# Performance work log

Hardware: AMD Instinct MI355X
Metric: run time of the kernel (lower is better)

Reference implementation:

```python
import jax, jax.numpy as jnp
import numpy as np

INT4_QMAX = 7.0  # symmetric int4: representable range clipped to [-8, 7]


def simulate_quantize_int4(w):
    # axis_to_reduce=None -> single global scale over the whole kernel
    scale = jnp.max(jnp.abs(w)) / INT4_QMAX
    q = jnp.clip(jnp.round(w / scale), -8.0, 7.0)
    return q * scale


def setup_inputs() -> dict:
    key = jax.random.key(0)
    k_x, k_w, k_bias, k_a, k_b = jax.random.split(key, 5)
    d_in, features, rank = 1024, 1024, 16
    x = jax.random.normal(k_x, (4, 8192, d_in), dtype=jnp.float32)
    kernel = jax.random.normal(k_w, (d_in, features), dtype=jnp.float32)
    bias = jax.random.normal(k_bias, (features,), dtype=jnp.float32)
    a = jax.random.normal(k_a, (d_in, rank), dtype=jnp.float32) * (1.0 / np.sqrt(d_in))
    b = jax.random.normal(k_b, (rank, features), dtype=jnp.float32) * 0.01
    return {"x": x, "kernel": kernel, "bias": bias, "a": a, "b": b}


def reference(x, kernel, bias, a, b):
    # fake-quantized main matmul: y = x @ dequant(quant(W)) + bias
    w = simulate_quantize_int4(kernel)
    y = jnp.einsum('bsd,df->bsf', x, w) + bias
    # LoRA adapter: x @ a @ b (contract small rank dim first)
    lora = jnp.einsum('bsr,rf->bsf', jnp.einsum('bsd,dr->bsr', x, a), b)
    return y + lora
```

## Files before the change

kernel.cpp:

```cpp
#include <hip/hip_runtime.h>
#include <hip/hip_bf16.h>

typedef __bf16 bf16x8 __attribute__((ext_vector_type(8)));
typedef __bf16 bf16x4 __attribute__((ext_vector_type(4)));
typedef float  f32x4  __attribute__((ext_vector_type(4)));

#define K_DIM 1024
#define N_DIM 1024
#define BM 128
#define BN 128
#define BK 64
#define BM2 256
#define BN2 256
#define BK2 32
#define NT2 (K_DIM / BK2)
#define AS_T (BM2 * BK2)
#define BS_T (BN2 * BK2)

typedef unsigned int u32;
typedef u32 __attribute__((address_space(1))) u32_g;
typedef u32 __attribute__((address_space(3))) u32_s;

__device__ __forceinline__ void load16_lds(const void* g, void* s) {
    __builtin_amdgcn_global_load_lds((u32_g*)g, (u32_s*)s, 16, 0, 0);
}

__global__ void maxabs_kernel(const float* __restrict__ w, float* __restrict__ blockmax, int n4) {
    __shared__ float sm[4];
    int i = blockIdx.x * blockDim.x + threadIdx.x;
    int stride = gridDim.x * blockDim.x;
    float m = 0.f;
    for (; i < n4; i += stride) {
        float4 v = ((const float4*)w)[i];
        m = fmaxf(m, fmaxf(fmaxf(fabsf(v.x), fabsf(v.y)), fmaxf(fabsf(v.z), fabsf(v.w))));
    }
#pragma unroll
    for (int off = 32; off > 0; off >>= 1)
        m = fmaxf(m, __shfl_down(m, off, 64));
    int lane = threadIdx.x & 63, wave = threadIdx.x >> 6;
    if (lane == 0) sm[wave] = m;
    __syncthreads();
    if (threadIdx.x == 0)
        blockmax[blockIdx.x] = fmaxf(fmaxf(sm[0], sm[1]), fmaxf(sm[2], sm[3]));
}

__global__ void build_w_kernel(const float* __restrict__ kern, const float* __restrict__ amat,
                               const float* __restrict__ bmat, const float* __restrict__ blockmax,
                               __bf16* __restrict__ wt) {
    __shared__ float smax;
    if (threadIdx.x < 64) {
        float m = 0.f;
#pragma unroll
        for (int j = 0; j < 4; ++j) m = fmaxf(m, blockmax[threadIdx.x + j * 64]);
#pragma unroll
        for (int off = 32; off > 0; off >>= 1)
            m = fmaxf(m, __shfl_down(m, off, 64));
        if (threadIdx.x == 0) smax = m;
    }
    __syncthreads();
    float scale = smax * (1.0f / 7.0f);

    int t = blockIdx.x * blockDim.x + threadIdx.x;
    int k = t & (K_DIM - 1);
    int n = t >> 10;
    float w = kern[k * N_DIM + n];
    float q = rintf(w / scale);
    q = fminf(fmaxf(q, -8.f), 7.f);
    float acc = q * scale;
#pragma unroll
    for (int r = 0; r < 16; ++r)
        acc += amat[k * 16 + r] * bmat[r * N_DIM + n];
    wt[(size_t)n * K_DIM + k] = (__bf16)acc;
}

__global__ __launch_bounds__(512, 2)
void gemm256_kernel(const float* __restrict__ x, const __bf16* __restrict__ wt,
                    const float* __restrict__ bias, float* __restrict__ out) {
    __shared__ __attribute__((aligned(16))) __bf16 As[2][AS_T];
    __shared__ __attribute__((aligned(16))) __bf16 Bs[4][BS_T];

    const int tid  = threadIdx.x;
    const int lane = tid & 63;
    const int wave = tid >> 6;
    const int wr   = wave >> 2;
    const int wc   = wave & 3;
    const int l15  = lane & 15;
    const int l4   = lane >> 4;

    const int lb  = blockIdx.x;
    const int ib  = lb >> 3;
    const int bn0 = (ib & 3) * BN2;
    const int bm0 = (((ib >> 2) << 3) | (lb & 7)) * BM2;

    const int srow = lane >> 2;
    const int lc   = (lane & 3) ^ ((srow >> 1) & 3);
    const __bf16* wg = wt + (size_t)(bn0 + wave * 32 + srow) * K_DIM + lc * 8;
    __bf16* sb = &Bs[0][wave * 32 * BK2];

    const int r0  = tid >> 3;
    const int c4  = tid & 7;
    const int apc = (c4 >> 1) ^ ((r0 >> 1) & 3);
    const int awr = r0 * BK2 + apc * 8 + (c4 & 1) * 4;
    const float* ag = x + (size_t)(bm0 + r0) * K_DIM + c4 * 4;

    const int ro = l15 * BK2 + ((l4 ^ ((l15 >> 1) & 3)) << 3);

    f32x4 acc[8][4] = {};
    float4 av0, av1, av2, av3;

#define STAGE_B(T) do { int b_ = (T) & 3; int k_ = ((T) & 31) * BK2;        \
        load16_lds(wg + k_,              sb + b_ * BS_T);                   \
        load16_lds(wg + 16 * K_DIM + k_, sb + b_ * BS_T + 16 * BK2); } while (0)

#define LOADA(T) do { const float* p_ = ag + ((T) & 31) * BK2;              \
        av0 = *(const float4*)(p_);                                         \
        av1 = *(const float4*)(p_ +  64 * K_DIM);                           \
        av2 = *(const float4*)(p_ + 128 * K_DIM);                           \
        av3 = *(const float4*)(p_ + 192 * K_DIM); } while (0)

#define WRITEA(T) do { __bf16* d_ = &As[(T) & 1][awr];                      \
        bf16x4 o0, o1, o2, o3;                                              \
        o0.x=(__bf16)av0.x; o0.y=(__bf16)av0.y; o0.z=(__bf16)av0.z; o0.w=(__bf16)av0.w; \
        o1.x=(__bf16)av1.x; o1.y=(__bf16)av1.y; o1.z=(__bf16)av1.z; o1.w=(__bf16)av1.w; \
        o2.x=(__bf16)av2.x; o2.y=(__bf16)av2.y; o2.z=(__bf16)av2.z; o2.w=(__bf16)av2.w; \
        o3.x=(__bf16)av3.x; o3.y=(__bf16)av3.y; o3.z=(__bf16)av3.z; o3.w=(__bf16)av3.w; \
        *(bf16x4*)(d_)        = o0;  *(bf16x4*)(d_ + 2048) = o1;            \
        *(bf16x4*)(d_ + 4096) = o2;  *(bf16x4*)(d_ + 6144) = o3; } while (0)

    LOADA(0);
    STAGE_B(0); STAGE_B(1); STAGE_B(2);
    asm volatile("s_waitcnt vmcnt(6)" ::: "memory");
    __builtin_amdgcn_sched_barrier(0);
    WRITEA(0);
    LOADA(1);
    asm volatile("s_waitcnt vmcnt(8)" ::: "memory");
    asm volatile("s_waitcnt lgkmcnt(0)" ::: "memory");
    __builtin_amdgcn_s_barrier();

#define ITER(t) do {                                                         \
        const int buf_ = (t) & 1; const int bbuf_ = (t) & 3;                 \
        const __bf16* ap = (const __bf16*)As + buf_ * AS_T + wr * (128 * BK2) + ro; \
        const __bf16* bp = (const __bf16*)Bs + bbuf_ * BS_T + wc * (64 * BK2) + ro; \
        bf16x8 af[8], bv[4];                                                 \
        af[0] = *(const bf16x8*)(ap + 0 * (16 * BK2));                       \
        af[1] = *(const bf16x8*)(ap + 1 * (16 * BK2));                       \
        af[2] = *(const bf16x8*)(ap + 2 * (16 * BK2));                       \
        af[3] = *(const bf16x8*)(ap + 3 * (16 * BK2));                       \
        bv[0] = *(const bf16x8*)(bp + 0 * (16 * BK2));                       \
        bv[1] = *(const bf16x8*)(bp + 1 * (16 * BK2));                       \
        af[4] = *(const bf16x8*)(ap + 4 * (16 * BK2));                       \
        af[5] = *(const bf16x8*)(ap + 5 * (16 * BK2));                       \
        af[6] = *(const bf16x8*)(ap + 6 * (16 * BK2));                       \
        af[7] = *(const bf16x8*)(ap + 7 * (16 * BK2));                       \
        bv[2] = *(const bf16x8*)(bp + 2 * (16 * BK2));                       \
        bv[3] = *(const bf16x8*)(bp + 3 * (16 * BK2));                       \
        STAGE_B((t) + 3);                                                    \
        asm volatile("s_waitcnt lgkmcnt(6)" ::: "memory");                   \
        __builtin_amdgcn_sched_barrier(0);                                   \
        __builtin_amdgcn_s_setprio(1);                                       \
        _Pragma("unroll") for (int mt = 0; mt < 4; ++mt)                     \
        _Pragma("unroll") for (int nt = 0; nt < 2; ++nt)                     \
            acc[mt][nt] = __builtin_amdgcn_mfma_f32_16x16x32_bf16(           \
                af[mt], bv[nt], acc[mt][nt], 0, 0, 0);                       \
        asm volatile("s_waitcnt lgkmcnt(2)" ::: "memory");                   \
        __builtin_amdgcn_sched_barrier(0);                                   \
        _Pragma("unroll") for (int mt = 4; mt < 8; ++mt)                     \
        _Pragma("unroll") for (int nt = 0; nt < 2; ++nt)                     \
            acc[mt][nt] = __builtin_amdgcn_mfma_f32_16x16x32_bf16(           \
                af[mt], bv[nt], acc[mt][nt], 0, 0, 0);                       \
        asm volatile("s_waitcnt vmcnt(2)" ::: "memory");                     \
        __builtin_amdgcn_sched_barrier(0);                                   \
        WRITEA((t) + 1);                                                     \
        LOADA((t) + 2);                                                      \
        asm volatile("s_waitcnt lgkmcnt(0)" ::: "memory");                   \
        __builtin_amdgcn_sched_barrier(0);                                   \
        _Pragma("unroll") for (int mt = 0; mt < 8; ++mt)                     \
        _Pragma("unroll") for (int nt = 2; nt < 4; ++nt)                     \
            acc[mt][nt] = __builtin_amdgcn_mfma_f32_16x16x32_bf16(           \
                af[mt], bv[nt], acc[mt][nt], 0, 0, 0);                       \
        __builtin_amdgcn_s_setprio(0);                                       \
        __builtin_amdgcn_s_barrier();                                        \
    } while (0)

#pragma unroll 4
    for (int t = 0; t < NT2; ++t) ITER(t);
#undef ITER
#undef STAGE_B
#undef LOADA
#undef WRITEA

#pragma unroll
    for (int nt = 0; nt < 4; ++nt) {
        int n = bn0 + wc * 64 + nt * 16 + l15;
        float bvs = bias[n];
#pragma unroll
        for (int mt = 0; mt < 8; ++mt) {
            int m = bm0 + wr * 128 + mt * 16 + l4 * 4;
            float* op = out + (size_t)m * N_DIM + n;
#pragma unroll
            for (int r = 0; r < 4; ++r)
                op[(size_t)r * N_DIM] = acc[mt][nt][r] + bvs;
        }
    }
}

__global__ __launch_bounds__(256, 4)
void gemm_fb_kernel(const float* __restrict__ x, const __bf16* __restrict__ wt,
                    const float* __restrict__ bias, float* __restrict__ out) {
    __shared__ __attribute__((aligned(16))) __bf16 As[BM * BK];
    __shared__ __attribute__((aligned(16))) __bf16 Bs[BN * BK];

    const int tid  = threadIdx.x;
    const int lane = tid & 63;
    const int wave = tid >> 6;
    const int wm = (wave >> 1) * 64;
    const int wn = (wave & 1) * 64;

    const int l = blockIdx.x;
    const int i = l >> 3;
    const int bn0 = (i & 7) * BN;
    const int bm0 = (((i >> 3) << 3) | (l & 7)) * BM;

    const int l15 = lane & 15;
    const int l4  = lane >> 4;

    f32x4 acc[4][4] = {};

    const int srow = lane >> 3;
    const int gch  = (lane & 7) ^ srow;

    for (int k0 = 0; k0 < K_DIM; k0 += BK) {
        __syncthreads();
#pragma unroll
        for (int j = 0; j < 4; ++j) {
            int r = j * 32 + wave * 8;
            const __bf16* g = wt + (size_t)(bn0 + r + srow) * K_DIM + k0 + gch * 8;
            load16_lds(g, &Bs[r * BK]);
        }
#pragma unroll
        for (int j = 0; j < 8; ++j) {
            int f  = j * 256 + tid;
            int r  = f >> 4;
            int c4 = f & 15;
            float4 v = *(const float4*)(x + (size_t)(bm0 + r) * K_DIM + k0 + c4 * 4);
            int p = (c4 >> 1) ^ (r & 7);
            bf16x4 o;
            o.x = (__bf16)v.x; o.y = (__bf16)v.y; o.z = (__bf16)v.z; o.w = (__bf16)v.w;
            *(bf16x4*)(&As[r * BK + p * 8 + (c4 & 1) * 4]) = o;
        }
        __syncthreads();

#pragma unroll
        for (int ks = 0; ks < 2; ++ks) {
            bf16x8 af[4], bfr[4];
#pragma unroll
            for (int mt = 0; mt < 4; ++mt) {
                int r = wm + mt * 16 + l15;
                int p = (ks * 4 + l4) ^ (r & 7);
                af[mt] = *(const bf16x8*)(&As[r * BK + p * 8]);
            }
#pragma unroll
            for (int nt = 0; nt < 4; ++nt) {
                int r = wn + nt * 16 + l15;
                int p = (ks * 4 + l4) ^ (r & 7);
                bfr[nt] = *(const bf16x8*)(&Bs[r * BK + p * 8]);
            }
#pragma unroll
            for (int mt = 0; mt < 4; ++mt)
#pragma unroll
                for (int nt = 0; nt < 4; ++nt)
                    acc[mt][nt] = __builtin_amdgcn_mfma_f32_16x16x32_bf16(
                        af[mt], bfr[nt], acc[mt][nt], 0, 0, 0);
        }
    }

#pragma unroll
    for (int nt = 0; nt < 4; ++nt) {
        int n = bn0 + wn + nt * 16 + l15;
        float bv = bias[n];
#pragma unroll
        for (int mt = 0; mt < 4; ++mt) {
            int m = bm0 + wm + mt * 16 + l4 * 4;
            float* op = out + (size_t)m * N_DIM + n;
#pragma unroll
            for (int r = 0; r < 4; ++r)
                op[(size_t)r * N_DIM] = acc[mt][nt][r] + bv;
        }
    }
}

extern "C" void kernel_launch(void* const* d_in, const int* in_sizes, int n_in,
                              void* d_out, int out_size, void* d_ws, size_t ws_size,
                              hipStream_t stream) {
    const float* x    = (const float*)d_in[0];
    const float* kern = (const float*)d_in[1];
    const float* bias = (const float*)d_in[2];
    const float* amat = (const float*)d_in[3];
    const float* bmat = (const float*)d_in[4];
    float* out = (float*)d_out;
    const int M = in_sizes[0] / K_DIM;

    float* blockmax = (float*)d_ws;
    __bf16* wt = (__bf16*)((char*)d_ws + 4096);
    const size_t need = 4096 + (size_t)N_DIM * K_DIM * sizeof(__bf16);
    (void)need;

    maxabs_kernel<<<256, 256, 0, stream>>>(kern, blockmax, K_DIM * N_DIM / 4);
    build_w_kernel<<<K_DIM * N_DIM / 256, 256, 0, stream>>>(kern, amat, bmat, blockmax, wt);

    if ((M % (BM2 * 8)) == 0) {
        gemm256_kernel<<<(M / BM2) * (N_DIM / BN2), 512, 0, stream>>>(x, wt, bias, out);
    } else {
        gemm_fb_kernel<<<(M / BM) * (N_DIM / BN), 256, 0, stream>>>(x, wt, bias, out);
    }
}
```

Before: 309.2 us.

## Stage fp32 activations directly into LDS via async loads and convert at fragment read

Replaces the register-staged load of fp32 x tiles (global load, convert to bf16, write LDS) with direct global_load_lds of fp32 data into a swizzled fp32 LDS buffer. Each wave now reads fp32 fragments from LDS and converts them to bf16 right before the MFMAs, interleaved with finer lgkmcnt waits. This removes VGPR staging and explicit LDS writes from the main loop, but doubles A-tile LDS footprint and LDS read traffic and adds per-iteration conversion work.

```diff
diff --git a/kernel.cpp b/kernel.cpp
--- a/kernel.cpp
+++ b/kernel.cpp
@@ -14,7 +14,7 @@
 #define BN2 256
 #define BK2 32
 #define NT2 (K_DIM / BK2)
-#define AS_T (BM2 * BK2)
+#define AS_F (BM2 * BK2)
 #define BS_T (BN2 * BK2)
 
 typedef unsigned int u32;
@@ -76,7 +76,7 @@
 __global__ __launch_bounds__(512, 2)
 void gemm256_kernel(const float* __restrict__ x, const __bf16* __restrict__ wt,
                     const float* __restrict__ bias, float* __restrict__ out) {
-    __shared__ __attribute__((aligned(16))) __bf16 As[2][AS_T];
+    __shared__ __attribute__((aligned(16))) float  AsF[2][AS_F];
     __shared__ __attribute__((aligned(16))) __bf16 Bs[4][BS_T];
 
     const int tid  = threadIdx.x;
@@ -97,97 +97,100 @@
     const __bf16* wg = wt + (size_t)(bn0 + wave * 32 + srow) * K_DIM + lc * 8;
     __bf16* sb = &Bs[0][wave * 32 * BK2];
 
-    const int r0  = tid >> 3;
-    const int c4  = tid & 7;
-    const int apc = (c4 >> 1) ^ ((r0 >> 1) & 3);
-    const int awr = r0 * BK2 + apc * 8 + (c4 & 1) * 4;
-    const float* ag = x + (size_t)(bm0 + r0) * K_DIM + c4 * 4;
-
-    const int ro = l15 * BK2 + ((l4 ^ ((l15 >> 1) & 3)) << 3);
+    const int ar  = wave * 32 + (lane >> 3);
+    const int ac  = (lane & 7) ^ (lane >> 3);
+    const float* xg = x + (size_t)(bm0 + ar) * K_DIM + ac * 4;
+    float* sa = &AsF[0][(wave * 32) * BK2];
+
+    const int ro  = l15 * BK2 + ((l4 ^ ((l15 >> 1) & 3)) << 3);
+    const int arow_off = (wr * 128 + l15) * BK2;
+    const int ap1 = ((l4 << 1) ^ (l15 & 7)) << 2;
 
     f32x4 acc[8][4] = {};
-    float4 av0, av1, av2, av3;
+
+#define STAGE_A(T) do { int s_ = (T) & 1; int k_ = ((T) & 31) * BK2;        \
+        const float* g_ = xg + k_; float* d_ = sa + s_ * AS_F;              \
+        load16_lds(g_,              d_);                                    \
+        load16_lds(g_ +  8 * K_DIM, d_ +  8 * BK2);                         \
+        load16_lds(g_ + 16 * K_DIM, d_ + 16 * BK2);                         \
+        load16_lds(g_ + 24 * K_DIM, d_ + 24 * BK2); } while (0)
 
 #define STAGE_B(T) do { int b_ = (T) & 3; int k_ = ((T) & 31) * BK2;        \
         load16_lds(wg + k_,              sb + b_ * BS_T);                   \
         load16_lds(wg + 16 * K_DIM + k_, sb + b_ * BS_T + 16 * BK2); } while (0)
 
-#define LOADA(T) do { const float* p_ = ag + ((T) & 31) * BK2;              \
-        av0 = *(const float4*)(p_);                                         \
-        av1 = *(const float4*)(p_ +  64 * K_DIM);                           \
-        av2 = *(const float4*)(p_ + 128 * K_DIM);                           \
-        av3 = *(const float4*)(p_ + 192 * K_DIM); } while (0)
-
-#define WRITEA(T) do { __bf16* d_ = &As[(T) & 1][awr];                      \
-        bf16x4 o0, o1, o2, o3;                                              \
-        o0.x=(__bf16)av0.x; o0.y=(__bf16)av0.y; o0.z=(__bf16)av0.z; o0.w=(__bf16)av0.w; \
-        o1.x=(__bf16)av1.x; o1.y=(__bf16)av1.y; o1.z=(__bf16)av1.z; o1.w=(__bf16)av1.w; \
-        o2.x=(__bf16)av2.x; o2.y=(__bf16)av2.y; o2.z=(__bf16)av2.z; o2.w=(__bf16)av2.w; \
-        o3.x=(__bf16)av3.x; o3.y=(__bf16)av3.y; o3.z=(__bf16)av3.z; o3.w=(__bf16)av3.w; \
-        *(bf16x4*)(d_)        = o0;  *(bf16x4*)(d_ + 2048) = o1;            \
-        *(bf16x4*)(d_ + 4096) = o2;  *(bf16x4*)(d_ + 6144) = o3; } while (0)
-
-    LOADA(0);
+#define RD_A(mt) do {                                                        \
+        uA[2*(mt)]   = *(const f32x4*)(ap + (mt) * (16 * BK2) + ap1);        \
+        uA[2*(mt)+1] = *(const f32x4*)(ap + (mt) * (16 * BK2) + (ap1 ^ 4));  \
+    } while (0)
+
+#define CVT_A(mt) do { f32x4 a_ = uA[2*(mt)], b_ = uA[2*(mt)+1]; bf16x8 t_;  \
+        t_[0]=(__bf16)a_[0]; t_[1]=(__bf16)a_[1];                            \
+        t_[2]=(__bf16)a_[2]; t_[3]=(__bf16)a_[3];                            \
+        t_[4]=(__bf16)b_[0]; t_[5]=(__bf16)b_[1];                            \
+        t_[6]=(__bf16)b_[2]; t_[7]=(__bf16)b_[3]; af[mt] = t_; } while (0)
+
+#define MF(mt, nt) acc[mt][nt] = __builtin_amdgcn_mfma_f32_16x16x32_bf16(    \
+        af[mt], bv[nt], acc[mt][nt], 0, 0, 0)
+
+    STAGE_A(0);
     STAGE_B(0); STAGE_B(1); STAGE_B(2);
-    asm volatile("s_waitcnt vmcnt(6)" ::: "memory");
-    __builtin_amdgcn_sched_barrier(0);
-    WRITEA(0);
-    LOADA(1);
-    asm volatile("s_waitcnt vmcnt(8)" ::: "memory");
-    asm volatile("s_waitcnt lgkmcnt(0)" ::: "memory");
+    asm volatile("s_waitcnt vmcnt(4)" ::: "memory");
     __builtin_amdgcn_s_barrier();
 
 #define ITER(t) do {                                                         \
-        const int buf_ = (t) & 1; const int bbuf_ = (t) & 3;                 \
-        const __bf16* ap = (const __bf16*)As + buf_ * AS_T + wr * (128 * BK2) + ro; \
-        const __bf16* bp = (const __bf16*)Bs + bbuf_ * BS_T + wc * (64 * BK2) + ro; \
-        bf16x8 af[8], bv[4];                                                 \
-        af[0] = *(const bf16x8*)(ap + 0 * (16 * BK2));                       \
-        af[1] = *(const bf16x8*)(ap + 1 * (16 * BK2));                       \
-        af[2] = *(const bf16x8*)(ap + 2 * (16 * BK2));                       \
-        af[3] = *(const bf16x8*)(ap + 3 * (16 * BK2));                       \
+        const int sa_ = (t) & 1; const int sb_ = (t) & 3;                    \
+        STAGE_A((t) + 1);                                                    \
+        const float*  ap = (const float*)AsF + sa_ * AS_F + arow_off;        \
+        const __bf16* bp = (const __bf16*)Bs + sb_ * BS_T + wc * (64 * BK2) + ro; \
+        f32x4 uA[16]; bf16x8 af[8], bv[4];                                   \
+        RD_A(0); RD_A(1);                                                    \
         bv[0] = *(const bf16x8*)(bp + 0 * (16 * BK2));                       \
         bv[1] = *(const bf16x8*)(bp + 1 * (16 * BK2));                       \
-        af[4] = *(const bf16x8*)(ap + 4 * (16 * BK2));                       \
-        af[5] = *(const bf16x8*)(ap + 5 * (16 * BK2));                       \
-        af[6] = *(const bf16x8*)(ap + 6 * (16 * BK2));                       \
-        af[7] = *(const bf16x8*)(ap + 7 * (16 * BK2));                       \
+        RD_A(2); RD_A(3);                                                    \
+        RD_A(4); RD_A(5);                                                    \
+        RD_A(6); RD_A(7);                                                    \
         bv[2] = *(const bf16x8*)(bp + 2 * (16 * BK2));                       \
         bv[3] = *(const bf16x8*)(bp + 3 * (16 * BK2));                       \
         STAGE_B((t) + 3);                                                    \
+        asm volatile("s_waitcnt lgkmcnt(14)" ::: "memory");                  \
+        __builtin_amdgcn_sched_barrier(0);                                   \
+        __builtin_amdgcn_s_setprio(1);                                       \
+        CVT_A(0); CVT_A(1);                                                  \
+        MF(0,0); MF(0,1); MF(1,0); MF(1,1);                                  \
+        asm volatile("s_waitcnt lgkmcnt(10)" ::: "memory");                  \
+        __builtin_amdgcn_sched_barrier(0);                                   \
+        CVT_A(2); CVT_A(3);                                                  \
+        MF(2,0); MF(2,1); MF(3,0); MF(3,1);                                  \
         asm volatile("s_waitcnt lgkmcnt(6)" ::: "memory");                   \
         __builtin_amdgcn_sched_barrier(0);                                   \
-        __builtin_amdgcn_s_setprio(1);                                       \
-        _Pragma("unroll") for (int mt = 0; mt < 4; ++mt)                     \
-        _Pragma("unroll") for (int nt = 0; nt < 2; ++nt)                     \
-            acc[mt][nt] = __builtin_amdgcn_mfma_f32_16x16x32_bf16(           \
-                af[mt], bv[nt], acc[mt][nt], 0, 0, 0);                       \
+        CVT_A(4); CVT_A(5);                                                  \
+        MF(4,0); MF(4,1); MF(5,0); MF(5,1);                                  \
         asm volatile("s_waitcnt lgkmcnt(2)" ::: "memory");                   \
         __builtin_amdgcn_sched_barrier(0);                                   \
-        _Pragma("unroll") for (int mt = 4; mt < 8; ++mt)                     \
-        _Pragma("unroll") for (int nt = 0; nt < 2; ++nt)                     \
-            acc[mt][nt] = __builtin_amdgcn_mfma_f32_16x16x32_bf16(           \
-                af[mt], bv[nt], acc[mt][nt], 0, 0, 0);                       \
+        CVT_A(6); CVT_A(7);                                                  \
+        MF(6,0); MF(6,1); MF(7,0); MF(7,1);                                  \
+        asm volatile("s_waitcnt lgkmcnt(0)" ::: "memory");                   \
+        __builtin_amdgcn_sched_barrier(0);                                   \
+        MF(0,2); MF(0,3); MF(1,2); MF(1,3);                                  \
+        MF(2,2); MF(2,3); MF(3,2); MF(3,3);                                  \
+        MF(4,2); MF(4,3); MF(5,2); MF(5,3);                                  \
+        MF(6,2); MF(6,3); MF(7,2); MF(7,3);                                  \
+        __builtin_amdgcn_s_setprio(0);                                       \
         asm volatile("s_waitcnt vmcnt(2)" ::: "memory");                     \
-        __builtin_amdgcn_sched_barrier(0);                                   \
-        WRITEA((t) + 1);                                                     \
-        LOADA((t) + 2);                                                      \
-        asm volatile("s_waitcnt lgkmcnt(0)" ::: "memory");                   \
-        __builtin_amdgcn_sched_barrier(0);                                   \
-        _Pragma("unroll") for (int mt = 0; mt < 8; ++mt)                     \
-        _Pragma("unroll") for (int nt = 2; nt < 4; ++nt)                     \
-            acc[mt][nt] = __builtin_amdgcn_mfma_f32_16x16x32_bf16(           \
-                af[mt], bv[nt], acc[mt][nt], 0, 0, 0);                       \
-        __builtin_amdgcn_s_setprio(0);                                       \
         __builtin_amdgcn_s_barrier();                                        \
     } while (0)
 
 #pragma unroll 4
     for (int t = 0; t < NT2; ++t) ITER(t);
 #undef ITER
+#undef STAGE_A
 #undef STAGE_B
-#undef LOADA
-#undef WRITEA
+#undef RD_A
+#undef CVT_A
+#undef MF
+
+    asm volatile("s_waitcnt vmcnt(0)" ::: "memory");
 
 #pragma unroll
     for (int nt = 0; nt < 4; ++nt) {
@@ -302,8 +305,6 @@
 
     float* blockmax = (float*)d_ws;
     __bf16* wt = (__bf16*)((char*)d_ws + 4096);
-    const size_t need = 4096 + (size_t)N_DIM * K_DIM * sizeof(__bf16);
-    (void)need;
 
     maxabs_kernel<<<256, 256, 0, stream>>>(kern, blockmax, K_DIM * N_DIM / 4);
     build_w_kernel<<<K_DIM * N_DIM / 256, 256, 0, stream>>>(kern, amat, bmat, blockmax, wt);
```

Measured after the change: 357.5 us. 15.6% more time.
